# Optimization experiments

Hardware: AMD Instinct MI355X
Metric: run time of the kernel (lower is better)

## Reference

```python
import jax, jax.numpy as jnp
import numpy as np

N, T = 4096, 1024
COND, PRED, PERIOD = 896, 56, 7


def setup_inputs() -> dict:
    key = jax.random.key(0)
    k1, k2 = jax.random.split(key)
    query = jax.random.normal(k1, (N, T), dtype=jnp.float32)
    # learned per-location params: [init_level, level_sm_logit, init_trend,
    #  trend_sm_logit, season_sm, period seasonality logits]
    params = 0.1 * jax.random.normal(k2, (N, 5 + PERIOD), dtype=jnp.float32)
    return {"query": query, "params": params}


def _forward(query, params):
    init_level = params[:, 0]                       # [N]
    level_sm = jax.nn.sigmoid(params[:, 1])         # [N]
    init_trend = params[:, 2]                       # [N]
    trend_sm = jax.nn.sigmoid(params[:, 3])         # [N]
    season_sm = params[:, 4]                        # NOTE: no sigmoid, matches original code
    init_seas = jax.nn.sigmoid(params[:, -PERIOD:])  # [N, PERIOD]

    def step(carry, y):
        prev_level, prev_trend, buf = carry          # buf: rolling window of last PERIOD seasonalities
        s_t = buf[:, 0]                              # seasonalities[t]
        pred = prev_level + prev_trend
        level = level_sm * y + (1.0 - level_sm) * pred
        diff = jnp.abs(level - prev_level)
        trend = trend_sm * (level - prev_level) + (1.0 - trend_sm) * prev_trend
        new_seas = season_sm * (y - pred) + (1.0 - season_sm) * s_t
        buf = jnp.concatenate([buf[:, 1:], new_seas[:, None]], axis=1)
        return (level, trend, buf), (level, trend, new_seas, diff)

    carry0 = (init_level, init_trend, init_seas)
    _, (levels, trends, new_seas_seq, diffs) = jax.lax.scan(step, carry0, query.T)
    levels = levels.T            # [N, T]
    trends = trends.T            # [N, T]
    new_seas_seq = new_seas_seq.T  # [N, T], == seasonalities[:, PERIOD:]
    level_diffs = diffs.T.mean(axis=1)  # [N]

    # full seasonality sequence: PERIOD initial values followed by T computed ones
    seas_full = jnp.concatenate([init_seas, new_seas_seq], axis=1)  # [N, PERIOD+T]

    sm = query - levels - new_seas_seq  # [N, T]

    horizon = jnp.arange(1, PRED + 1, dtype=levels.dtype)  # [PRED]
    last_levels = levels[:, COND - 1:, None]   # [N, W, 1], W = T-COND+1
    last_trends = trends[:, COND - 1:, None]
    pr = last_levels + last_trends * horizon   # [N, W, PRED]

    # cyclic seasonality forecast per window
    season_index = jnp.tile(jnp.arange(PERIOD), (PRED + PERIOD - 1) // PERIOD)[:PRED]
    starts = jnp.arange(COND, T + 1)           # [W]
    idx = starts[:, None] + season_index[None, :]  # [W, PRED]
    pr = pr + seas_full[:, idx]                # [N, W, PRED]

    return sm, pr, level_diffs


def reference(query, params):
    return _forward(query, params)
```

## Files before the change

### kernel.cpp

```cpp
#include <hip/hip_runtime.h>
#include <cmath>

#define NROWS 4096
#define TLEN  1024
#define RPB   8
#define LT0   895
#define ST0   889
#define LTN   129
#define STN   135
#define PRV4R 1806
#define PRV4B (RPB * PRV4R)

__device__ __forceinline__ float sigmoidf_(float x) {
    return 1.0f / (1.0f + expf(-x));
}

__device__ __forceinline__ float f4c(const float4& v, int k) {
    switch (k & 3) { case 0: return v.x; case 1: return v.y; case 2: return v.z; default: return v.w; }
}

#define PR_EMIT(qv_)                                                          \
    {                                                                         \
        const int q_   = (qv_);                                               \
        const int row_ = q_ / PRV4R;                                          \
        const int rem_ = q_ - row_ * PRV4R;                                   \
        const int s_   = rem_ / 14;                                           \
        const int h4_  = rem_ - s_ * 14;                                      \
        const float L_ = Ltl[row_ * 132 + s_];                                \
        const float T_ = Ttl[row_ * 132 + s_];                                \
        const float* stp_ = &Stl[row_ * 136 + s_];                            \
        const int hb_ = h4_ * 4;                                              \
        int m0_ = hb_ % 7;                                                    \
        int m1_ = m0_ + 1; if (m1_ >= 7) m1_ -= 7;                            \
        int m2_ = m1_ + 1; if (m2_ >= 7) m2_ -= 7;                            \
        int m3_ = m2_ + 1; if (m3_ >= 7) m3_ -= 7;                            \
        const float hbf_ = (float)hb_;                                        \
        float4 o_;                                                            \
        o_.x = fmaf(T_, hbf_ + 1.0f, L_) + stp_[m0_];                         \
        o_.y = fmaf(T_, hbf_ + 2.0f, L_) + stp_[m1_];                         \
        o_.z = fmaf(T_, hbf_ + 3.0f, L_) + stp_[m2_];                         \
        o_.w = fmaf(T_, hbf_ + 4.0f, L_) + stp_[m3_];                         \
        prb[q_] = o_;                                                         \
    }

__global__ __launch_bounds__(512, 4)
void es_fused(const float* __restrict__ query,
              const float* __restrict__ params,
              float* __restrict__ sm,
              float* __restrict__ diffs,
              float4* __restrict__ pr4)
{
    __shared__ float4 ystage[RPB * 256];
    __shared__ float lds_P[RPB * 65];
    __shared__ float lds_start[RPB * 65];
    __shared__ float lds_q[RPB * 225];
    __shared__ float lds_dsum[RPB * 33];
    __shared__ float lds_par[RPB * 16];
    __shared__ float Ltl[RPB * 132];
    __shared__ float Ttl[RPB * 132];
    __shared__ float Stl[RPB * 136];

    const int tid = threadIdx.x;
    const int base = blockIdx.x * RPB;
    const int r = (tid >> 5) & 7;
    const int k = tid & 31;
    const int n = base + r;

    {
        const float4* qb = reinterpret_cast<const float4*>(query + (size_t)base * TLEN);
        #pragma unroll
        for (int i = 0; i < 4; ++i) {
            const int w = i * 512 + tid;
            ystage[(w & ~7) | ((w ^ (w >> 3)) & 7)] = qb[w];
        }
    }

    float a = 0.f, b = 0.f, c = 0.f, ia = 0.f, ib = 0.f, ic = 0.f;
    if (tid < 256) {
        const float* pp = params + (size_t)n * 12;
        a  = sigmoidf_(pp[1]);
        b  = sigmoidf_(pp[3]);
        c  = pp[4];
        ia = 1.0f - a; ib = 1.0f - b; ic = 1.0f - c;
        if (k == 0) {
            float* par = &lds_par[r * 16];
            par[0] = pp[0];
            par[1] = pp[2];
            par[2] = ia;
            par[3] = -(a * b);
            par[4] = ib + b * ia;
            par[5] = ic;
            #pragma unroll
            for (int l = 0; l < 7; ++l) par[6 + l] = sigmoidf_(pp[5 + l]);
        }
    }
    __syncthreads();

    float4 yv[8];
    float e[32];
    float st0 = 0.f, st1 = 0.f;

    if (tid < 256) {
        const int ksw = k & 7;
        #pragma unroll
        for (int i = 0; i < 8; ++i)
            yv[i] = ystage[r * 256 + ((k * 8 + i) ^ ksw)];

        float L = 0.0f, B = 0.0f;
        #pragma unroll
        for (int j = 0; j < 32; ++j) {
            const float yy = f4c(yv[j >> 2], j);
            const float pred  = L + B;
            const float level = fmaf(a, yy, ia * pred);
            const float trend = fmaf(b, level - L, ib * B);
            L = level; B = trend;
        }
        lds_P[r * 65 + 2 * k]     = L;
        lds_P[r * 65 + 2 * k + 1] = B;
    }
    __syncthreads();

    if (tid < 8) {
        const float* par = &lds_par[tid * 16];
        float m00 = par[2], m01 = par[2], m10 = par[3], m11 = par[4];
        #pragma unroll
        for (int s = 0; s < 5; ++s) {
            const float t00 = m00 * m00 + m01 * m10;
            const float t01 = m00 * m01 + m01 * m11;
            const float t10 = m10 * m00 + m11 * m10;
            const float t11 = m10 * m01 + m11 * m11;
            m00 = t00; m01 = t01; m10 = t10; m11 = t11;
        }
        float P0[32], P1[32];
        #pragma unroll
        for (int kk = 0; kk < 32; ++kk) {
            P0[kk] = lds_P[tid * 65 + 2 * kk];
            P1[kk] = lds_P[tid * 65 + 2 * kk + 1];
        }
        float s0 = par[0], s1 = par[1];
        #pragma unroll
        for (int kk = 0; kk < 32; ++kk) {
            lds_start[tid * 65 + 2 * kk]     = s0;
            lds_start[tid * 65 + 2 * kk + 1] = s1;
            const float t0 = m00 * s0 + m01 * s1 + P0[kk];
            const float t1 = m10 * s0 + m11 * s1 + P1[kk];
            s0 = t0; s1 = t1;
        }
    }
    __syncthreads();

    if (tid < 256) {
        st0 = lds_start[r * 65 + 2 * k];
        st1 = lds_start[r * 65 + 2 * k + 1];
        float L = st0, B = st1, dsum = 0.0f;
        float q[7] = {0,0,0,0,0,0,0};
        #pragma unroll
        for (int j = 0; j < 32; ++j) {
            const float yy = f4c(yv[j >> 2], j);
            const float pred  = L + B;
            const float level = fmaf(a, yy, ia * pred);
            const float d     = level - L;
            dsum += fabsf(d);
            const float trend = fmaf(b, d, ib * B);
            const float ee    = yy - pred;
            e[j] = ee;
            q[j % 7] = fmaf(ic, q[j % 7], c * ee);
            L = level; B = trend;
        }
        const int kp = (4 * k) % 7;
        #pragma unroll
        for (int l = 0; l < 7; ++l) {
            int g = kp + l; if (g >= 7) g -= 7;
            lds_q[r * 225 + k * 7 + g] = q[l];
        }
        lds_dsum[r * 33 + k] = dsum;

        if (k >= 27) {
            float prevL = st0, Bv = st1;
            #pragma unroll
            for (int j = 0; j < 32; ++j) {
                const float level = f4c(yv[j >> 2], j) - ia * e[j];
                const float trend = fmaf(b, level - prevL, ib * Bv);
                const int tg = k * 32 + j;
                if (tg >= LT0) {
                    Ltl[r * 132 + tg - LT0] = level;
                    Ttl[r * 132 + tg - LT0] = trend;
                }
                prevL = level; Bv = trend;
            }
        }
    }
    __syncthreads();

    if (tid < 56) {
        const int rr = tid / 7, p = tid % 7;
        const float icc = lds_par[rr * 16 + 5];
        const float ic2 = icc * icc;
        const float ic4 = ic2 * ic2;
        const float ic5 = ic4 * icc;
        float v = lds_par[rr * 16 + 6 + p];
        float qq[32];
        #pragma unroll
        for (int kk = 0; kk < 32; ++kk) qq[kk] = lds_q[rr * 225 + kk * 7 + p];
        int l = p;
        #pragma unroll
        for (int kk = 0; kk < 32; ++kk) {
            const float m = (l < 4) ? ic5 : ic4;
            const float nv = fmaf(m, v, qq[kk]);
            lds_q[rr * 225 + kk * 7 + p] = v;
            v = nv;
            l += 3; if (l >= 7) l -= 7;
        }
    } else if (tid < 64) {
        const int rr = tid - 56;
        float s = 0.0f;
        #pragma unroll
        for (int kk = 0; kk < 32; ++kk) s += lds_dsum[rr * 33 + kk];
        diffs[blockIdx.x * RPB + rr] = s * (1.0f / 1024.0f);
    }
    __syncthreads();

    if (tid < 256 && k >= 27) {
        float sg[7];
        const int kp = (4 * k) % 7;
        #pragma unroll
        for (int l = 0; l < 7; ++l) {
            int g = kp + l; if (g >= 7) g -= 7;
            sg[l] = lds_q[r * 225 + k * 7 + g];
        }
        #pragma unroll
        for (int j = 0; j < 32; ++j) {
            const float sn = fmaf(ic, sg[j % 7], c * e[j]);
            sg[j % 7] = sn;
            const int tg = k * 32 + j;
            if (tg >= ST0) Stl[r * 136 + tg - ST0] = sn;
        }
    }
    __syncthreads();

    float4* prb = pr4 + (size_t)blockIdx.x * PRV4B;

    if (tid >= 256) {
        const int u = tid - 256;
        #pragma unroll 4
        for (int i = 0; i < 32; ++i) {
            PR_EMIT(i * 256 + u);
        }
    } else {
        {
            float sg[7];
            const int kp = (4 * k) % 7;
            #pragma unroll
            for (int l = 0; l < 7; ++l) {
                int g = kp + l; if (g >= 7) g -= 7;
                sg[l] = lds_q[r * 225 + k * 7 + g];
            }
            float4 ov;
            float* smrow = sm + (size_t)n * TLEN + k * 32;
            #pragma unroll
            for (int j = 0; j < 32; ++j) {
                const float sn = fmaf(ic, sg[j % 7], c * e[j]);
                sg[j % 7] = sn;
                const float smv = ia * e[j] - sn;
                switch (j & 3) { case 0: ov.x = smv; break; case 1: ov.y = smv; break;
                                 case 2: ov.z = smv; break; default: ov.w = smv; }
                if ((j & 3) == 3)
                    *reinterpret_cast<float4*>(smrow + (j - 3)) = ov;
            }
        }
        #pragma unroll 4
        for (int i = 0; i < 24; ++i) {
            PR_EMIT(8192 + i * 256 + tid);
        }
        if (tid < 112) {
            PR_EMIT(8192 + 6144 + tid);
        }
    }
}

extern "C" void kernel_launch(void* const* d_in, const int* in_sizes, int n_in,
                              void* d_out, int out_size, void* d_ws, size_t ws_size,
                              hipStream_t stream) {
    const float* query  = (const float*)d_in[0];
    const float* params = (const float*)d_in[1];

    float* out   = (float*)d_out;
    float* sm    = out;
    float* pr    = out + (size_t)NROWS * TLEN;
    float* diffs = pr  + (size_t)NROWS * 129 * 56;

    hipLaunchKernelGGL(es_fused, dim3(NROWS / RPB), dim3(512), 0, stream,
                       query, params, sm, diffs, (float4*)pr);
}
```

Baseline: 37.41 us.

## Stage sm rows through LDS for coalesced nontemporal stores and rebalance pr emission

The seasonal recurrence is now computed once per thread, and the sm values go into an XOR-swizzled LDS staging buffer. After a barrier, all 512 threads write sm for the block's rows as contiguous float4 nontemporal stores. The pr output is split evenly across all threads instead of favouring the upper half, and it also uses nontemporal stores. Launch bounds drop from 4 to 2 blocks per CU, which gives the compiler more register room but may lower occupancy.

Result: no change. 37.86 us (+1.2%).

```diff
diff --git a/kernel.cpp b/kernel.cpp
--- a/kernel.cpp
+++ b/kernel.cpp
@@ -11,12 +11,19 @@
 #define PRV4R 1806
 #define PRV4B (RPB * PRV4R)
 
+typedef float f32x4 __attribute__((ext_vector_type(4)));
+
 __device__ __forceinline__ float sigmoidf_(float x) {
     return 1.0f / (1.0f + expf(-x));
 }
 
 __device__ __forceinline__ float f4c(const float4& v, int k) {
     switch (k & 3) { case 0: return v.x; case 1: return v.y; case 2: return v.z; default: return v.w; }
+}
+
+__device__ __forceinline__ void nt_store4(float4* p, const float4& v) {
+    f32x4 t; t.x = v.x; t.y = v.y; t.z = v.z; t.w = v.w;
+    __builtin_nontemporal_store(t, reinterpret_cast<f32x4*>(p));
 }
 
 #define PR_EMIT(qv_)                                                          \
@@ -40,10 +47,10 @@
         o_.y = fmaf(T_, hbf_ + 2.0f, L_) + stp_[m1_];                         \
         o_.z = fmaf(T_, hbf_ + 3.0f, L_) + stp_[m2_];                         \
         o_.w = fmaf(T_, hbf_ + 4.0f, L_) + stp_[m3_];                         \
-        prb[q_] = o_;                                                         \
-    }
-
-__global__ __launch_bounds__(512, 4)
+        nt_store4(&prb[q_], o_);                                              \
+    }
+
+__global__ __launch_bounds__(512, 2)
 void es_fused(const float* __restrict__ query,
               const float* __restrict__ params,
               float* __restrict__ sm,
@@ -220,7 +227,7 @@
     }
     __syncthreads();
 
-    if (tid < 256 && k >= 27) {
+    if (tid < 256) {
         float sg[7];
         const int kp = (4 * k) % 7;
         #pragma unroll
@@ -228,52 +235,48 @@
             int g = kp + l; if (g >= 7) g -= 7;
             sg[l] = lds_q[r * 225 + k * 7 + g];
         }
+        const int ksw = k & 7;
+        float4 ov;
         #pragma unroll
         for (int j = 0; j < 32; ++j) {
             const float sn = fmaf(ic, sg[j % 7], c * e[j]);
             sg[j % 7] = sn;
-            const int tg = k * 32 + j;
-            if (tg >= ST0) Stl[r * 136 + tg - ST0] = sn;
-        }
-    }
-    __syncthreads();
-
-    float4* prb = pr4 + (size_t)blockIdx.x * PRV4B;
-
-    if (tid >= 256) {
-        const int u = tid - 256;
-        #pragma unroll 4
-        for (int i = 0; i < 32; ++i) {
-            PR_EMIT(i * 256 + u);
-        }
-    } else {
-        {
-            float sg[7];
-            const int kp = (4 * k) % 7;
-            #pragma unroll
-            for (int l = 0; l < 7; ++l) {
-                int g = kp + l; if (g >= 7) g -= 7;
-                sg[l] = lds_q[r * 225 + k * 7 + g];
-            }
-            float4 ov;
-            float* smrow = sm + (size_t)n * TLEN + k * 32;
+            const float smv = ia * e[j] - sn;
+            e[j] = sn;
+            switch (j & 3) { case 0: ov.x = smv; break; case 1: ov.y = smv; break;
+                             case 2: ov.z = smv; break; default: ov.w = smv; }
+            if ((j & 3) == 3)
+                ystage[r * 256 + ((k * 8 + (j >> 2)) ^ ksw)] = ov;
+        }
+        if (k >= 27) {
             #pragma unroll
             for (int j = 0; j < 32; ++j) {
-                const float sn = fmaf(ic, sg[j % 7], c * e[j]);
-                sg[j % 7] = sn;
-                const float smv = ia * e[j] - sn;
-                switch (j & 3) { case 0: ov.x = smv; break; case 1: ov.y = smv; break;
-                                 case 2: ov.z = smv; break; default: ov.w = smv; }
-                if ((j & 3) == 3)
-                    *reinterpret_cast<float4*>(smrow + (j - 3)) = ov;
+                const int tg = k * 32 + j;
+                if (tg >= ST0) Stl[r * 136 + tg - ST0] = e[j];
             }
         }
+    }
+    __syncthreads();
+
+    {
+        float4* smb = reinterpret_cast<float4*>(sm + (size_t)base * TLEN);
+        #pragma unroll
+        for (int i = 0; i < 4; ++i) {
+            const int w = i * 512 + tid;
+            const float4 v = ystage[(w & ~7) | ((w ^ (w >> 3)) & 7)];
+            nt_store4(&smb[w], v);
+        }
+    }
+
+    {
+        float4* prb = pr4 + (size_t)blockIdx.x * PRV4B;
         #pragma unroll 4
-        for (int i = 0; i < 24; ++i) {
-            PR_EMIT(8192 + i * 256 + tid);
-        }
-        if (tid < 112) {
-            PR_EMIT(8192 + 6144 + tid);
+        for (int i = 0; i < 28; ++i) {
+            PR_EMIT(i * 512 + tid);
+        }
+        const int q = 28 * 512 + tid;
+        if (q < PRV4B) {
+            PR_EMIT(q);
         }
     }
 }
```
